# Optimization experiments

Hardware: AMD Instinct MI355X
Metric: run time of the kernel (lower is better)

## Reference

```python
import jax, jax.numpy as jnp
import numpy as np

N_EMBD = 1024
BLOCK_SIZE = 128
HEAD_SIZE = 128
THETA = 10000.0


def setup_inputs() -> dict:
    key = jax.random.key(0)
    k1, k2, k3, k4 = jax.random.split(key, 4)
    B, T = 256, BLOCK_SIZE
    x = jax.random.normal(k1, (B, T, N_EMBD), dtype=jnp.float32)
    # nn.Linear(n_embd, head_size, bias=False) stored as [n_embd, head_size] so y = x @ W
    s = 1.0 / np.sqrt(N_EMBD)
    Wq = jax.random.normal(k2, (N_EMBD, HEAD_SIZE), dtype=jnp.float32) * s
    Wk = jax.random.normal(k3, (N_EMBD, HEAD_SIZE), dtype=jnp.float32) * s
    Wv = jax.random.normal(k4, (N_EMBD, HEAD_SIZE), dtype=jnp.float32) * s
    return {"x": x, "Wq": Wq, "Wk": Wk, "Wv": Wv}


def _rope_cos_sin(T: int, head_size: int):
    # freqs = exp(arange(0, hs, 2) * (-log(theta)/hs)); angles = outer(t, freqs)
    inv_freq = jnp.exp(jnp.arange(0, head_size, 2, dtype=jnp.float32) * (-np.log(THETA) / head_size))
    angles = jnp.arange(T, dtype=jnp.float32)[:, None] * inv_freq[None, :]  # [T, hs/2]
    return jnp.cos(angles), jnp.sin(angles)


def _apply_rope(t, cos, sin):
    # complex-view rotation on interleaved (even, odd) pairs of the last dim
    tr = t[..., 0::2]  # real parts  [B,T,hs/2]
    ti = t[..., 1::2]  # imag parts
    out_r = tr * cos - ti * sin
    out_i = tr * sin + ti * cos
    return jnp.stack([out_r, out_i], axis=-1).reshape(t.shape)


def reference(x, Wq, Wk, Wv):
    B, T, _ = x.shape
    hs = Wq.shape[1]
    q = x @ Wq  # [B,T,hs]
    k = x @ Wk
    v = x @ Wv
    cos, sin = _rope_cos_sin(T, hs)
    q = _apply_rope(q, cos, sin)
    k = _apply_rope(k, cos, sin)
    scores = jnp.einsum('btd,bsd->bts', q, k) / jnp.sqrt(jnp.asarray(hs, q.dtype))
    causal = jnp.tril(jnp.ones((T, T), dtype=bool))
    scores = jnp.where(causal[None, :, :], scores, -jnp.inf)
    att = jax.nn.softmax(scores, axis=-1)  # dropout is identity in eval
    return jnp.einsum('bts,bsd->btd', att, v)
```

## Files before the change

### kernel.cpp

```cpp
#include <hip/hip_runtime.h>
#include <math.h>

typedef __bf16 bf16x8 __attribute__((ext_vector_type(8)));
typedef float  f32x4  __attribute__((ext_vector_type(4)));
typedef unsigned short us4 __attribute__((ext_vector_type(4)));

constexpr int N_EMBD = 1024;
constexpr int T_SEQ  = 128;
constexpr int HS     = 128;
constexpr int BATCH  = 256;
constexpr int ROWS   = BATCH * T_SEQ;

__device__ __forceinline__ void async16(const void* g, void* l) {
    __builtin_amdgcn_global_load_lds(
        (const __attribute__((address_space(1))) unsigned int*)g,
        (__attribute__((address_space(3))) unsigned int*)l, 16, 0, 0);
}
__device__ __forceinline__ unsigned short bfbits(float f) {
    return __builtin_bit_cast(unsigned short, (__bf16)f);
}
__device__ __forceinline__ f32x4 zero4() {
    f32x4 z = {0.f, 0.f, 0.f, 0.f};
    return z;
}

__global__ __launch_bounds__(256) void wcast(
    const float* __restrict__ Wq, const float* __restrict__ Wk,
    const float* __restrict__ Wv, unsigned short* __restrict__ Wt)
{
    __shared__ unsigned short tile[64][130];
    const int bid = blockIdx.x;
    const int nt  = bid >> 4;
    const int k0  = (bid & 15) << 6;
    const float* src = (nt == 0) ? Wq : ((nt == 1) ? Wk : Wv);
    const int tid = threadIdx.x;
#pragma unroll
    for (int j = 0; j < 32; ++j) {
        int idx = tid + j * 256;
        int k = idx >> 7, n = idx & 127;
        tile[k][n] = bfbits(src[(size_t)(k0 + k) * HS + n]);
    }
    __syncthreads();
#pragma unroll
    for (int j = 0; j < 32; ++j) {
        int idx = tid + j * 256;
        int n = idx >> 6, kk = idx & 63;
        Wt[(size_t)(nt * 128 + n) * N_EMBD + k0 + kk] = tile[kk][n];
    }
}

__global__ __launch_bounds__(512, 2) void head_fused(
    const float* __restrict__ x,
    const unsigned short* __restrict__ Wt,
    float* __restrict__ out)
{
    __shared__ char lds[139264];
    constexpr int QS = 0;
    constexpr int KS = 34816;
    constexpr int VS = 69632;
    constexpr int STG_A = 104448;
    constexpr int STG_B = 114688;

    const int tid  = threadIdx.x;
    const int w    = tid >> 6;
    const int l    = tid & 63;
    const int cl   = l & 15;
    const int quad = l >> 4;
    const int b    = blockIdx.x;
    const int row0 = b << 7;
    const int wm   = (w & 1) << 6;
    const int wn   = (w >> 1) * 96;

    const int arow = tid >> 2;
    const int acol = (tid & 3) << 3;
    const float* aptr = x + (size_t)(row0 + arow) * N_EMBD + acol;
    const int bsrc = (l & 3) ^ quad;

    f32x4 acc[4][6];
#pragma unroll
    for (int a = 0; a < 4; ++a)
#pragma unroll
        for (int c = 0; c < 6; ++c) acc[a][c] = zero4();

    f32x4 a0 = *(const f32x4*)(aptr);
    f32x4 a1 = *(const f32x4*)(aptr + 4);

    for (int kc = 0; kc < N_EMBD; kc += 32) {
        __syncthreads();
        bf16x8 aw;
        aw[0] = (__bf16)a0[0]; aw[1] = (__bf16)a0[1];
        aw[2] = (__bf16)a0[2]; aw[3] = (__bf16)a0[3];
        aw[4] = (__bf16)a1[0]; aw[5] = (__bf16)a1[1];
        aw[6] = (__bf16)a1[2]; aw[7] = (__bf16)a1[3];
        *(bf16x8*)(lds + STG_A + arow * 80 + (tid & 3) * 16) = aw;
#pragma unroll
        for (int jj = 0; jj < 3; ++jj) {
            int j = w * 3 + jj;
            int n = j * 16 + (l >> 2);
            async16(Wt + (size_t)n * N_EMBD + kc + bsrc * 8,
                    lds + STG_B + j * 1024 + 0);
        }
        __syncthreads();
        if (kc + 32 < N_EMBD) {
            a0 = *(const f32x4*)(aptr + kc + 32);
            a1 = *(const f32x4*)(aptr + kc + 36);
        }
        bf16x8 af[4], bf[6];
#pragma unroll
        for (int rt = 0; rt < 4; ++rt) {
            int m = wm + rt * 16 + cl;
            af[rt] = *(const bf16x8*)(lds + STG_A + m * 80 + quad * 16);
        }
#pragma unroll
        for (int ct = 0; ct < 6; ++ct) {
            int n = wn + ct * 16 + cl;
            bf[ct] = *(const bf16x8*)(lds + STG_B + n * 64 + ((quad ^ ((n >> 2) & 3)) << 4));
        }
#pragma unroll
        for (int rt = 0; rt < 4; ++rt)
#pragma unroll
            for (int ct = 0; ct < 6; ++ct)
                acc[rt][ct] = __builtin_amdgcn_mfma_f32_16x16x32_bf16(
                    af[rt], bf[ct], acc[rt][ct], 0, 0, 0);
    }

    const float LNT = 0.07195578430905272f;
#pragma unroll
    for (int ct = 0; ct < 6; ++ct) {
        int c0  = wn + ct * 16;
        int ntc = c0 >> 7;
        int d   = (c0 & 127) + cl;
        if (ntc < 2) {
            int qk = (ntc == 0) ? QS : KS;
            float freq = __expf(-(float)(d & ~1) * LNT);
#pragma unroll
            for (int rt = 0; rt < 4; ++rt) {
#pragma unroll
                for (int i = 0; i < 4; ++i) {
                    int t = wm + rt * 16 + quad * 4 + i;
                    float v = acc[rt][ct][i];
                    float p = __shfl_xor(v, 1);
                    float sn, cs;
                    __sincosf((float)t * freq, &sn, &cs);
                    float r = ((d & 1) == 0) ? (v * cs - p * sn) : (p * sn + v * cs);
                    *(unsigned short*)(lds + qk + t * 272 + d * 2) = bfbits(r);
                }
            }
        } else {
#pragma unroll
            for (int rt = 0; rt < 4; ++rt) {
                int s0 = wm + rt * 16 + quad * 4;
                us4 u;
                u.x = bfbits(acc[rt][ct][0]);
                u.y = bfbits(acc[rt][ct][1]);
                u.z = bfbits(acc[rt][ct][2]);
                u.w = bfbits(acc[rt][ct][3]);
                *(us4*)(lds + VS + d * 272 + s0 * 2) = u;
            }
        }
    }
    __syncthreads();

    const int nct = w + 1;
    const int nks = (w + 2) >> 1;
    char* pl = lds + STG_A + w * 4352;

    bf16x8 qf[4];
#pragma unroll
    for (int ks = 0; ks < 4; ++ks)
        qf[ks] = *(const bf16x8*)(lds + QS + (w * 16 + cl) * 272 + (ks * 4 + quad) * 16);

    f32x4 s[8];
#pragma unroll
    for (int ct = 0; ct < 8; ++ct) s[ct] = zero4();

#pragma unroll
    for (int ct = 0; ct < 8; ++ct) if (ct < nct) {
        const char* kr = lds + KS + (ct * 16 + cl) * 272;
#pragma unroll
        for (int ks = 0; ks < 4; ++ks) {
            bf16x8 bb = *(const bf16x8*)(kr + (ks * 4 + quad) * 16);
            s[ct] = __builtin_amdgcn_mfma_f32_16x16x32_bf16(qf[ks], bb, s[ct], 0, 0, 0);
        }
    }

    const float scale = 0.08838834764831845f;
#pragma unroll
    for (int i = 0; i < 4; ++i) {
        int t = w * 16 + quad * 4 + i;
        float mx = -3.0e38f;
#pragma unroll
        for (int ct = 0; ct < 8; ++ct) if (ct < nct) {
            int col = ct * 16 + cl;
            float v = s[ct][i] * scale;
            v = (col <= t) ? v : -INFINITY;
            s[ct][i] = v;
            mx = fmaxf(mx, v);
        }
        mx = fmaxf(mx, __shfl_xor(mx, 1));
        mx = fmaxf(mx, __shfl_xor(mx, 2));
        mx = fmaxf(mx, __shfl_xor(mx, 4));
        mx = fmaxf(mx, __shfl_xor(mx, 8));
        float sum = 0.f;
#pragma unroll
        for (int ct = 0; ct < 8; ++ct) if (ct < nct) {
            float p = __expf(s[ct][i] - mx);
            s[ct][i] = p;
            sum += p;
        }
        sum += __shfl_xor(sum, 1);
        sum += __shfl_xor(sum, 2);
        sum += __shfl_xor(sum, 4);
        sum += __shfl_xor(sum, 8);
        float inv = 1.0f / sum;
        int rl = quad * 4 + i;
#pragma unroll
        for (int ct = 0; ct < 8; ++ct) if (ct < nct) {
            *(unsigned short*)(pl + rl * 272 + (ct * 16 + cl) * 2) =
                bfbits(s[ct][i] * inv);
        }
        if ((w & 1) == 0) {
            *(unsigned short*)(pl + rl * 272 + (nct * 16 + cl) * 2) = 0;
        }
    }

    bf16x8 ap[4];
#pragma unroll
    for (int ks = 0; ks < 4; ++ks) if (ks < nks)
        ap[ks] = *(const bf16x8*)(pl + cl * 272 + (ks * 4 + quad) * 16);

    f32x4 o[8];
#pragma unroll
    for (int ct = 0; ct < 8; ++ct) o[ct] = zero4();

#pragma unroll
    for (int ct = 0; ct < 8; ++ct) {
        const char* vr = lds + VS + (ct * 16 + cl) * 272;
#pragma unroll
        for (int ks = 0; ks < 4; ++ks) if (ks < nks) {
            bf16x8 bb = *(const bf16x8*)(vr + (ks * 4 + quad) * 16);
            o[ct] = __builtin_amdgcn_mfma_f32_16x16x32_bf16(ap[ks], bb, o[ct], 0, 0, 0);
        }
    }

#pragma unroll
    for (int ct = 0; ct < 8; ++ct)
#pragma unroll
        for (int i = 0; i < 4; ++i) {
            int t = w * 16 + quad * 4 + i;
            out[(size_t)b * 16384 + (size_t)t * HS + ct * 16 + cl] = o[ct][i];
        }
}

extern "C" void kernel_launch(void* const* d_in, const int* in_sizes, int n_in,
                              void* d_out, int out_size, void* d_ws, size_t ws_size,
                              hipStream_t stream) {
    const float* x  = (const float*)d_in[0];
    const float* Wq = (const float*)d_in[1];
    const float* Wk = (const float*)d_in[2];
    const float* Wv = (const float*)d_in[3];
    float* out = (float*)d_out;

    unsigned short* Wt = (unsigned short*)d_ws;

    wcast<<<48, 256, 0, stream>>>(Wq, Wk, Wv, Wt);
    head_fused<<<BATCH, 512, 0, stream>>>(x, Wt, out);
}
```

Baseline: 226.4 us.

## Double-buffer QKV projection mainloop with 64-wide K chunks and XOR swizzle

Result: no change. 227.3 us (+0.4%).

```diff
diff --git a/kernel.cpp b/kernel.cpp
--- a/kernel.cpp
+++ b/kernel.cpp
@@ -9,7 +9,6 @@
 constexpr int T_SEQ  = 128;
 constexpr int HS     = 128;
 constexpr int BATCH  = 256;
-constexpr int ROWS   = BATCH * T_SEQ;
 
 __device__ __forceinline__ void async16(const void* g, void* l) {
     __builtin_amdgcn_global_load_lds(
@@ -55,11 +54,12 @@
     float* __restrict__ out)
 {
     __shared__ char lds[139264];
+    constexpr int AB0 = 0,     AB1 = 16384;
+    constexpr int BB0 = 32768, BB1 = 81920;
     constexpr int QS = 0;
     constexpr int KS = 34816;
     constexpr int VS = 69632;
-    constexpr int STG_A = 104448;
-    constexpr int STG_B = 114688;
+    constexpr int PS = 104448;
 
     const int tid  = threadIdx.x;
     const int w    = tid >> 6;
@@ -72,9 +72,12 @@
     const int wn   = (w >> 1) * 96;
 
     const int arow = tid >> 2;
-    const int acol = (tid & 3) << 3;
-    const float* aptr = x + (size_t)(row0 + arow) * N_EMBD + acol;
-    const int bsrc = (l & 3) ^ quad;
+    const int acq  = tid & 3;
+    const float* aptr = x + (size_t)(row0 + arow) * N_EMBD + acq * 16;
+    const int as0 = (acq * 2) ^ (arow & 7);
+    const int as1 = (acq * 2 + 1) ^ (arow & 7);
+    const int brow_lo = l >> 3;
+    const int bswz = ((l & 7) ^ (l >> 3)) * 8;
 
     f32x4 acc[4][6];
 #pragma unroll
@@ -82,46 +85,89 @@
 #pragma unroll
         for (int c = 0; c < 6; ++c) acc[a][c] = zero4();
 
-    f32x4 a0 = *(const f32x4*)(aptr);
-    f32x4 a1 = *(const f32x4*)(aptr + 4);
-
-    for (int kc = 0; kc < N_EMBD; kc += 32) {
+    f32x4 ar[2][4];
+
+#define LOAD_A(set, chunk)                                             \
+    do {                                                               \
+        const float* p_ = aptr + (chunk) * 64;                         \
+        ar[set][0] = *(const f32x4*)(p_);                              \
+        ar[set][1] = *(const f32x4*)(p_ + 4);                          \
+        ar[set][2] = *(const f32x4*)(p_ + 8);                          \
+        ar[set][3] = *(const f32x4*)(p_ + 12);                         \
+    } while (0)
+
+#define STAGE_A(dst, set)                                              \
+    do {                                                               \
+        bf16x8 w0_, w1_;                                               \
+        w0_[0] = (__bf16)ar[set][0][0]; w0_[1] = (__bf16)ar[set][0][1];\
+        w0_[2] = (__bf16)ar[set][0][2]; w0_[3] = (__bf16)ar[set][0][3];\
+        w0_[4] = (__bf16)ar[set][1][0]; w0_[5] = (__bf16)ar[set][1][1];\
+        w0_[6] = (__bf16)ar[set][1][2]; w0_[7] = (__bf16)ar[set][1][3];\
+        w1_[0] = (__bf16)ar[set][2][0]; w1_[1] = (__bf16)ar[set][2][1];\
+        w1_[2] = (__bf16)ar[set][2][2]; w1_[3] = (__bf16)ar[set][2][3];\
+        w1_[4] = (__bf16)ar[set][3][0]; w1_[5] = (__bf16)ar[set][3][1];\
+        w1_[6] = (__bf16)ar[set][3][2]; w1_[7] = (__bf16)ar[set][3][3];\
+        *(bf16x8*)(lds + (dst) + arow * 128 + (as0 << 4)) = w0_;       \
+        *(bf16x8*)(lds + (dst) + arow * 128 + (as1 << 4)) = w1_;       \
+    } while (0)
+
+#define ASYNC_B(dst, chunk)                                            \
+    do {                                                               \
+        _Pragma("unroll")                                              \
+        for (int jj_ = 0; jj_ < 6; ++jj_) {                            \
+            int j_ = w * 6 + jj_;                                      \
+            int n_ = j_ * 8 + brow_lo;                                 \
+            async16(Wt + (size_t)n_ * N_EMBD + (chunk) * 64 + bswz,    \
+                    lds + (dst) + j_ * 1024);                          \
+        }                                                              \
+    } while (0)
+
+#define COMPUTE(ca, cb)                                                \
+    do {                                                               \
+        _Pragma("unroll")                                              \
+        for (int ks_ = 0; ks_ < 2; ++ks_) {                            \
+            const int kq_ = ks_ * 4 + quad;                            \
+            bf16x8 af_[4], bf_[6];                                     \
+            _Pragma("unroll")                                          \
+            for (int rt_ = 0; rt_ < 4; ++rt_) {                        \
+                int m_ = wm + rt_ * 16 + cl;                           \
+                af_[rt_] = *(const bf16x8*)(lds + (ca) + m_ * 128 +    \
+                                            ((kq_ ^ (m_ & 7)) << 4));  \
+            }                                                          \
+            _Pragma("unroll")                                          \
+            for (int ct_ = 0; ct_ < 6; ++ct_) {                        \
+                int n_ = wn + ct_ * 16 + cl;                           \
+                bf_[ct_] = *(const bf16x8*)(lds + (cb) + n_ * 128 +    \
+                                            ((kq_ ^ (n_ & 7)) << 4));  \
+            }                                                          \
+            _Pragma("unroll")                                          \
+            for (int rt_ = 0; rt_ < 4; ++rt_)                          \
+                _Pragma("unroll")                                      \
+                for (int ct_ = 0; ct_ < 6; ++ct_)                      \
+                    acc[rt_][ct_] = __builtin_amdgcn_mfma_f32_16x16x32_bf16( \
+                        af_[rt_], bf_[ct_], acc[rt_][ct_], 0, 0, 0);   \
+        }                                                              \
+    } while (0)
+
+    LOAD_A(0, 0);
+    STAGE_A(AB0, 0);
+    ASYNC_B(BB0, 0);
+    LOAD_A(1, 1);
+    __syncthreads();
+
+#pragma unroll
+    for (int it = 0; it < 16; ++it) {
+        const int curA = (it & 1) ? AB1 : AB0;
+        const int nxtA = (it & 1) ? AB0 : AB1;
+        const int curB = (it & 1) ? BB1 : BB0;
+        const int nxtB = (it & 1) ? BB0 : BB1;
+        if (it < 15) {
+            ASYNC_B(nxtB, it + 1);
+            STAGE_A(nxtA, (it + 1) & 1);
+            if (it < 14) LOAD_A(it & 1, it + 2);
+        }
+        COMPUTE(curA, curB);
         __syncthreads();
-        bf16x8 aw;
-        aw[0] = (__bf16)a0[0]; aw[1] = (__bf16)a0[1];
-        aw[2] = (__bf16)a0[2]; aw[3] = (__bf16)a0[3];
-        aw[4] = (__bf16)a1[0]; aw[5] = (__bf16)a1[1];
-        aw[6] = (__bf16)a1[2]; aw[7] = (__bf16)a1[3];
-        *(bf16x8*)(lds + STG_A + arow * 80 + (tid & 3) * 16) = aw;
-#pragma unroll
-        for (int jj = 0; jj < 3; ++jj) {
-            int j = w * 3 + jj;
-            int n = j * 16 + (l >> 2);
-            async16(Wt + (size_t)n * N_EMBD + kc + bsrc * 8,
-                    lds + STG_B + j * 1024 + 0);
-        }
-        __syncthreads();
-        if (kc + 32 < N_EMBD) {
-            a0 = *(const f32x4*)(aptr + kc + 32);
-            a1 = *(const f32x4*)(aptr + kc + 36);
-        }
-        bf16x8 af[4], bf[6];
-#pragma unroll
-        for (int rt = 0; rt < 4; ++rt) {
-            int m = wm + rt * 16 + cl;
-            af[rt] = *(const bf16x8*)(lds + STG_A + m * 80 + quad * 16);
-        }
-#pragma unroll
-        for (int ct = 0; ct < 6; ++ct) {
-            int n = wn + ct * 16 + cl;
-            bf[ct] = *(const bf16x8*)(lds + STG_B + n * 64 + ((quad ^ ((n >> 2) & 3)) << 4));
-        }
-#pragma unroll
-        for (int rt = 0; rt < 4; ++rt)
-#pragma unroll
-            for (int ct = 0; ct < 6; ++ct)
-                acc[rt][ct] = __builtin_amdgcn_mfma_f32_16x16x32_bf16(
-                    af[rt], bf[ct], acc[rt][ct], 0, 0, 0);
     }
 
     const float LNT = 0.07195578430905272f;
@@ -163,7 +209,7 @@
 
     const int nct = w + 1;
     const int nks = (w + 2) >> 1;
-    char* pl = lds + STG_A + w * 4352;
+    char* pl = lds + PS + w * 4352;
 
     bf16x8 qf[4];
 #pragma unroll
@@ -250,6 +296,10 @@
             int t = w * 16 + quad * 4 + i;
             out[(size_t)b * 16384 + (size_t)t * HS + ct * 16 + cl] = o[ct][i];
         }
+#undef LOAD_A
+#undef STAGE_A
+#undef ASYNC_B
+#undef COMPUTE
 }
 
 extern "C" void kernel_launch(void* const* d_in, const int* in_sizes, int n_in,
```
